# Performance work log

Measured on AMD Instinct MI355X. Metric: run time of the kernel, lower is better.

The kernel has to match this reference:

```python
import jax, jax.numpy as jnp
import numpy as np

SEQ, B, OBS, H, MLP_H, ACT = 64, 8192, 47, 64, 32, 12


def setup_inputs() -> dict:
    key = jax.random.key(0)
    ks = jax.random.split(key, 10)
    s = 1.0 / np.sqrt(H)
    return {
        "obs_seq": jax.random.normal(ks[0], (SEQ, B, OBS), dtype=jnp.float32),
        "h0": jnp.zeros((1, B, H), jnp.float32),
        "c0": jnp.zeros((1, B, H), jnp.float32),
        "W_ih": jax.random.uniform(ks[1], (4 * H, OBS), jnp.float32, -s, s),
        "W_hh": jax.random.uniform(ks[2], (4 * H, H), jnp.float32, -s, s),
        "b_ih": jax.random.uniform(ks[3], (4 * H,), jnp.float32, -s, s),
        "b_hh": jax.random.uniform(ks[4], (4 * H,), jnp.float32, -s, s),
        "W1": jax.random.uniform(ks[5], (MLP_H, H), jnp.float32, -s, s),
        "b1": jax.random.uniform(ks[6], (MLP_H,), jnp.float32, -s, s),
        "W2": jax.random.uniform(ks[7], (ACT, MLP_H), jnp.float32, -0.1, 0.1),
        "b2": jnp.zeros((ACT,), jnp.float32),
        "masks": jax.random.randint(ks[8], (SEQ, B), 0, 2, dtype=jnp.int32),
    }


def _lstm_scan(obs_seq, h0, c0, W_ih, W_hh, b_ih, b_hh, masks):
    b = b_ih + b_hh

    def step(carry, inp):
        h, c = carry  # (B,H)
        x, m = inp
        m = m.astype(h.dtype)[:, None]  # (B,1): 0 resets hidden state
        h = h * m
        c = c * m
        gates = x @ W_ih.T + h @ W_hh.T + b  # (B,4H), torch order i,f,g,o
        i, f, g, o = jnp.split(gates, 4, axis=-1)
        c = jax.nn.sigmoid(f) * c + jax.nn.sigmoid(i) * jnp.tanh(g)
        h = jax.nn.sigmoid(o) * jnp.tanh(c)
        return (h, c), h

    (h, c), outs = jax.lax.scan(step, (h0[0], c0[0]), (obs_seq, masks))
    return outs, h, c


def reference(obs_seq, h0, c0, W_ih, W_hh, b_ih, b_hh, W1, b1, W2, b2, masks):
    lstm_out, h, c = _lstm_scan(obs_seq, h0, c0, W_ih, W_hh, b_ih, b_hh, masks)
    means = jax.nn.elu(lstm_out @ W1.T + b1) @ W2.T + b2  # (SEQ,B,ACT)
    return means, h[None], c[None]
```

## Files before the change

### kernel.cpp

```cpp
#include <hip/hip_runtime.h>
#include <hip/hip_bf16.h>

#define SEQ   64
#define BATCH 8192
#define OBS   47
#define HID   64
#define MLPH  32
#define ACT   12

#define BT 16
#define NT 512
#define NWG (BATCH / BT)

#define XS0O 0
#define XS1O 2048
#define HM0O 4096
#define HM1O 6144
#define XA0O 8192
#define XA1O 24576
#define M2EO 40960
#define MSKO 43008
#define W1LO 47104
#define W2LO 51200
#define SMEM_BYTES 52224

#define L2E  1.4426950408889634f
#define L2E2 2.8853900817779268f

typedef __attribute__((ext_vector_type(8))) short short8;
typedef __attribute__((ext_vector_type(4))) float f32x4;

__device__ __forceinline__ ushort f2bf(float f) {
  union { float f; unsigned u; } v; v.f = f;
  return (ushort)((v.u + 0x7FFFu + ((v.u >> 16) & 1u)) >> 16);
}
__device__ __forceinline__ float ex2(float x) {
#if __has_builtin(__builtin_amdgcn_exp2f)
  return __builtin_amdgcn_exp2f(x);
#else
  return __expf(x * 0.6931471805599453f);
#endif
}
__device__ __forceinline__ float rcpx(float x) {
#if __has_builtin(__builtin_amdgcn_rcpf)
  return __builtin_amdgcn_rcpf(x);
#else
  return __fdividef(1.0f, x);
#endif
}
__device__ __forceinline__ float sigf(float x)     { return rcpx(1.0f + ex2(-L2E * x)); }
__device__ __forceinline__ float tanhfast(float x) { return __builtin_fmaf(-2.0f, rcpx(1.0f + ex2(L2E2 * x)), 1.0f); }
__device__ __forceinline__ unsigned cvtpk(float lo, float hi) {
  unsigned r; asm("v_cvt_pk_bf16_f32 %0, %1, %2" : "=v"(r) : "v"(lo), "v"(hi)); return r;
}

__device__ __forceinline__ void barrier_lgkm() {
  __builtin_amdgcn_sched_barrier(0);
  asm volatile("s_waitcnt lgkmcnt(0)" ::: "memory");
  __builtin_amdgcn_s_barrier();
  __builtin_amdgcn_sched_barrier(0);
}

__device__ __forceinline__ int swz (int r, int ks) { return (r * 128 + ks * 2) ^ ((r & 7) << 4); }
__device__ __forceinline__ int swzM(int r, int cs) { return (r * 64  + cs * 2) ^ ((r & 7) << 4); }

extern "C" __global__ void __launch_bounds__(NT, 4)
lstm_policy(const float* __restrict__ obs, const float* __restrict__ h0,
            const float* __restrict__ c0, const float* __restrict__ Wih,
            const float* __restrict__ Whh, const float* __restrict__ bih,
            const float* __restrict__ bhh, const float* __restrict__ W1,
            const float* __restrict__ b1, const float* __restrict__ W2,
            const float* __restrict__ b2, const int* __restrict__ masks,
            float* __restrict__ out)
{
  __shared__ __align__(16) char sm[SMEM_BYTES];
  const int tid  = threadIdx.x;
  const int b0   = blockIdx.x * BT;
  const int lane = tid & 63;
  const int w    = tid >> 6;
  const int lr   = lane & 15;
  const int lg   = lane >> 4;
  const int j    = (w & 3) * 16 + lr;

  int xsl[4];
  #pragma unroll
  for (int nf = 0; nf < 4; ++nf)
    xsl[nf] = (j << 8) + ((((lg * 4 + nf) ^ lr) & 15) << 4);

  for (int idx = tid; idx < 256; idx += NT)
    *(f32x4*)(sm + idx * 16) = (f32x4){0.f, 0.f, 0.f, 0.f};
  for (int idx = tid; idx < SEQ * BT; idx += NT) {
    int t = idx >> 4, r = idx & 15;
    *(float*)(sm + MSKO + idx * 4) = (float)masks[t * BATCH + b0 + r];
  }
  if (tid < 64) {
    int l = tid, llr = l & 15, llg = l >> 4;
    #pragma unroll
    for (int tt = 0; tt < 2; ++tt)
      #pragma unroll
      for (int kk = 0; kk < 2; ++kk) {
        short8 f;
        const float* src = W1 + (tt * 16 + llr) * HID + kk * 32 + llg * 8;
        #pragma unroll
        for (int e = 0; e < 8; ++e) f[e] = (short)f2bf(src[e]);
        *(short8*)(sm + W1LO + ((tt * 2 + kk) * 64 + l) * 16) = f;
      }
    short8 f2;
    #pragma unroll
    for (int e = 0; e < 8; ++e)
      f2[e] = (llr < ACT) ? (short)f2bf(W2[llr * MLPH + llg * 8 + e]) : (short)0;
    *(short8*)(sm + W2LO + l * 16) = f2;
  }
  __syncthreads();

  short8 wf[4][2];
  float biasg[4] = {0, 0, 0, 0};
  float creg[4] = {0, 0, 0, 0}, hlast[4] = {0, 0, 0, 0};
  int shw[4];
  #pragma unroll
  for (int q = 0; q < 4; ++q) shw[q] = swz(lg * 4 + q, j);

  if (w < 4) {
    #pragma unroll
    for (int nf = 0; nf < 4; ++nf) {
      int n = nf * 64 + j;
      #pragma unroll
      for (int kk = 0; kk < 2; ++kk) {
        const float* src = Whh + n * HID + kk * 32 + lg * 8;
        short8 f;
        #pragma unroll
        for (int e = 0; e < 8; ++e) f[e] = (short)f2bf(src[e]);
        wf[nf][kk] = f;
      }
    }
    #pragma unroll
    for (int q = 0; q < 4; ++q) {
      int r = lg * 4 + q;
      creg[q] = c0[(size_t)(b0 + r) * HID + j];
      *(ushort*)(sm + HM0O + shw[q]) = f2bf(h0[(size_t)(b0 + r) * HID + j]);
    }
  } else {
    #pragma unroll
    for (int nf = 0; nf < 4; ++nf) {
      int n = nf * 64 + j;
      biasg[nf] = bih[n] + bhh[n];
      #pragma unroll
      for (int kk = 0; kk < 2; ++kk) {
        short8 f;
        #pragma unroll
        for (int e = 0; e < 8; ++e) {
          int k = kk * 32 + lg * 8 + e;
          f[e] = (k < OBS) ? (short)f2bf(Wih[n * OBS + k]) : (short)0;
        }
        wf[nf][kk] = f;
      }
    }
  }

  float b1v0 = 0.f, b1v1 = 0.f, b2v = 0.f;
  if (w == 4) { b1v0 = b1[lr]; b1v1 = b1[16 + lr]; }
  if (w == 5) { b2v = (lr < ACT) ? b2[lr] : 0.f; }

  const int oidx = tid - 320;
  const bool oact = (w >= 5) && (oidx >= 0) && (oidx < 188);
  int a_obs[4] = {0, 0, 0, 0};
  f32x4 ovh = {0.f, 0.f, 0.f, 0.f};
  const float* obsp = obs;
  if (oact) {
    #pragma unroll
    for (int e = 0; e < 4; ++e) {
      int flat = oidx * 4 + e;
      int r = flat / OBS, k = flat - OBS * r;
      a_obs[e] = swz(r, k);
    }
    f32x4 v0 = *(const f32x4*)(obs + (size_t)b0 * OBS + oidx * 4);
    f32x4 v1 = *(const f32x4*)(obs + ((size_t)BATCH + b0) * OBS + oidx * 4);
    #pragma unroll
    for (int e = 0; e < 4; ++e) *(ushort*)(sm + XS0O + a_obs[e]) = f2bf(v0[e]);
    #pragma unroll
    for (int e = 0; e < 4; ++e) *(ushort*)(sm + XS1O + a_obs[e]) = f2bf(v1[e]);
    obsp = obs + ((size_t)2 * BATCH + b0) * OBS + oidx * 4;
    ovh = *(const f32x4*)(obsp);
    obsp += (size_t)BATCH * OBS;
  }
  __syncthreads();

  auto do_xgemm = [&](int B) {
    const int xsb = B ? XS1O : XS0O;
    const int xab = B ? XA1O : XA0O;
    short8 ax0 = *(const short8*)(sm + xsb + swz(lr, lg * 8));
    short8 ax1 = *(const short8*)(sm + xsb + swz(lr, 32 + lg * 8));
    #pragma unroll
    for (int nf = 0; nf < 4; ++nf) {
      f32x4 a = (f32x4){biasg[nf], biasg[nf], biasg[nf], biasg[nf]};
      a = __builtin_amdgcn_mfma_f32_16x16x32_bf16(ax0, wf[nf][0], a, 0, 0, 0);
      a = __builtin_amdgcn_mfma_f32_16x16x32_bf16(ax1, wf[nf][1], a, 0, 0, 0);
      *(f32x4*)(sm + xab + xsl[nf]) = a;
    }
  };

  if (w >= 4) do_xgemm(0);
  __syncthreads();

  auto do_mlp1 = [&](int TT, int HMB) {
    const int me = M2EO + (TT & 1) * 1024;
    short8 hf0 = *(const short8*)(sm + HMB + swz(lr, lg * 8));
    short8 hf1 = *(const short8*)(sm + HMB + swz(lr, 32 + lg * 8));
    f32x4 am0 = (f32x4){b1v0, b1v0, b1v0, b1v0};
    f32x4 am1 = (f32x4){b1v1, b1v1, b1v1, b1v1};
    short8 wA;
    wA = *(const short8*)(sm + W1LO + (0 * 64 + lane) * 16);
    am0 = __builtin_amdgcn_mfma_f32_16x16x32_bf16(hf0, wA, am0, 0, 0, 0);
    wA = *(const short8*)(sm + W1LO + (1 * 64 + lane) * 16);
    am0 = __builtin_amdgcn_mfma_f32_16x16x32_bf16(hf1, wA, am0, 0, 0, 0);
    wA = *(const short8*)(sm + W1LO + (2 * 64 + lane) * 16);
    am1 = __builtin_amdgcn_mfma_f32_16x16x32_bf16(hf0, wA, am1, 0, 0, 0);
    wA = *(const short8*)(sm + W1LO + (3 * 64 + lane) * 16);
    am1 = __builtin_amdgcn_mfma_f32_16x16x32_bf16(hf1, wA, am1, 0, 0, 0);
    #pragma unroll
    for (int q = 0; q < 4; ++q) {
      int r = lg * 4 + q;
      float v0 = am0[q], v1 = am1[q];
      float e0 = v0 > 0.f ? v0 : (ex2(L2E * v0) - 1.f);
      float e1 = v1 > 0.f ? v1 : (ex2(L2E * v1) - 1.f);
      unsigned u = cvtpk(e0, e1);
      *(ushort*)(sm + me + swzM(r, lr))      = (ushort)u;
      *(ushort*)(sm + me + swzM(r, 16 + lr)) = (ushort)(u >> 16);
    }
  };

  auto do_mlp2 = [&](int TT) {
    const int me = M2EO + (TT & 1) * 1024;
    f32x4 a2 = (f32x4){b2v, b2v, b2v, b2v};
    short8 ef  = *(const short8*)(sm + me + swzM(lr, lg * 8));
    short8 w2f = *(const short8*)(sm + W2LO + lane * 16);
    a2 = __builtin_amdgcn_mfma_f32_16x16x32_bf16(ef, w2f, a2, 0, 0, 0);
    if (lr < ACT) {
      float* op = out + ((size_t)TT * BATCH + b0 + lg * 4) * ACT + lr;
      #pragma unroll
      for (int q = 0; q < 4; ++q) op[q * ACT] = a2[q];
    }
  };

  auto do_step = [&](int P, int T) {
    if (w < 4) {
      __builtin_amdgcn_s_setprio(1);
      const int hmr = P ? HM1O : HM0O;
      const int hmw = P ? HM0O : HM1O;
      const int xar = P ? XA1O : XA0O;
      short8 ah0 = *(const short8*)(sm + hmr + swz(lr, lg * 8));
      short8 ah1 = *(const short8*)(sm + hmr + swz(lr, 32 + lg * 8));
      f32x4 xq0 = *(const f32x4*)(sm + xar + xsl[0]);
      f32x4 xq1 = *(const f32x4*)(sm + xar + xsl[1]);
      f32x4 xq2 = *(const f32x4*)(sm + xar + xsl[2]);
      f32x4 xq3 = *(const f32x4*)(sm + xar + xsl[3]);
      const f32x4 z = {0.f, 0.f, 0.f, 0.f};
      f32x4 pa0 = __builtin_amdgcn_mfma_f32_16x16x32_bf16(ah0, wf[0][0], z, 0, 0, 0);
      f32x4 pa1 = __builtin_amdgcn_mfma_f32_16x16x32_bf16(ah0, wf[1][0], z, 0, 0, 0);
      f32x4 pa2 = __builtin_amdgcn_mfma_f32_16x16x32_bf16(ah0, wf[2][0], z, 0, 0, 0);
      f32x4 pa3 = __builtin_amdgcn_mfma_f32_16x16x32_bf16(ah0, wf[3][0], z, 0, 0, 0);
      f32x4 pb0 = __builtin_amdgcn_mfma_f32_16x16x32_bf16(ah1, wf[0][1], z, 0, 0, 0);
      f32x4 pb1 = __builtin_amdgcn_mfma_f32_16x16x32_bf16(ah1, wf[1][1], z, 0, 0, 0);
      f32x4 pb2 = __builtin_amdgcn_mfma_f32_16x16x32_bf16(ah1, wf[2][1], z, 0, 0, 0);
      f32x4 pb3 = __builtin_amdgcn_mfma_f32_16x16x32_bf16(ah1, wf[3][1], z, 0, 0, 0);

      f32x4 mc = *(const f32x4*)(sm + MSKO + (T << 6) + (lg << 4));
      f32x4 g0 = xq0 + mc * (pa0 + pb0);
      f32x4 g1 = xq1 + mc * (pa1 + pb1);
      f32x4 g2 = xq2 + mc * (pa2 + pb2);
      f32x4 g3 = xq3 + mc * (pa3 + pb3);

      float hq[4];
      #pragma unroll
      for (int q = 0; q < 4; ++q) {
        float iv = sigf(g0[q]);
        float fv = sigf(g1[q]);
        float gv = tanhfast(g2[q]);
        float ov = sigf(g3[q]);
        float c  = fv * (creg[q] * mc[q]) + iv * gv;
        float h  = ov * tanhfast(c);
        creg[q]  = c;
        hlast[q] = h;
        hq[q]    = h;
      }
      unsigned u01 = cvtpk(hq[0], hq[1]);
      unsigned u23 = cvtpk(hq[2], hq[3]);
      *(ushort*)(sm + hmw + shw[0]) = (ushort)u01;
      *(ushort*)(sm + hmw + shw[1]) = (ushort)(u01 >> 16);
      *(ushort*)(sm + hmw + shw[2]) = (ushort)u23;
      *(ushort*)(sm + hmw + shw[3]) = (ushort)(u23 >> 16);
      __builtin_amdgcn_s_setprio(0);
    } else {
      if (T + 1 < SEQ) do_xgemm(P ^ 1);
      if (w == 4) {
        if (T > 0) do_mlp1(T - 1, P ? HM1O : HM0O);
      } else if (w == 5 && T > 1) {
        do_mlp2(T - 2);
      }
      if (oact) {
        f32x4 ovn = ovh;
        if (T + 3 < SEQ) { ovn = *(const f32x4*)(obsp); }
        obsp += (size_t)BATCH * OBS;
        if (T + 2 < SEQ) {
          const int xsw = P ? XS1O : XS0O;
          unsigned p0 = cvtpk(ovh[0], ovh[1]), p1 = cvtpk(ovh[2], ovh[3]);
          *(ushort*)(sm + xsw + a_obs[0]) = (ushort)p0;
          *(ushort*)(sm + xsw + a_obs[1]) = (ushort)(p0 >> 16);
          *(ushort*)(sm + xsw + a_obs[2]) = (ushort)p1;
          *(ushort*)(sm + xsw + a_obs[3]) = (ushort)(p1 >> 16);
        }
        ovh = ovn;
      }
    }
    barrier_lgkm();
  };

  for (int t = 0; t < SEQ; t += 2) {
    do_step(0, t);
    do_step(1, t + 1);
  }
  if (w == 4) do_mlp1(63, HM0O);
  else if (w == 5) do_mlp2(62);
  barrier_lgkm();
  if (w == 5) do_mlp2(63);

  if (w < 4) {
    float* hout = out + (size_t)SEQ * BATCH * ACT;
    float* cout = hout + (size_t)BATCH * HID;
    #pragma unroll
    for (int q = 0; q < 4; ++q) {
      int r = lg * 4 + q;
      hout[(size_t)(b0 + r) * HID + j] = hlast[q];
      cout[(size_t)(b0 + r) * HID + j] = creg[q];
    }
  }
}

extern "C" void kernel_launch(void* const* d_in, const int* in_sizes, int n_in,
                              void* d_out, int out_size, void* d_ws, size_t ws_size,
                              hipStream_t stream) {
  (void)in_sizes; (void)n_in; (void)d_ws; (void)ws_size; (void)out_size;
  lstm_policy<<<dim3(NWG), dim3(NT), 0, stream>>>(
      (const float*)d_in[0], (const float*)d_in[1], (const float*)d_in[2],
      (const float*)d_in[3], (const float*)d_in[4], (const float*)d_in[5],
      (const float*)d_in[6], (const float*)d_in[7], (const float*)d_in[8],
      (const float*)d_in[9], (const float*)d_in[10], (const int*)d_in[11],
      (float*)d_out);
}
```

Before: 106.8 us.

## Merge helper waves into recurrent waves, halving workgroup size to 256 threads

New measurement: 109.5 us. 1.03x slower.

```diff
diff --git a/kernel.cpp b/kernel.cpp
--- a/kernel.cpp
+++ b/kernel.cpp
@@ -9,7 +9,7 @@
 #define ACT   12
 
 #define BT 16
-#define NT 512
+#define NT 256
 #define NWG (BATCH / BT)
 
 #define XS0O 0
@@ -64,7 +64,7 @@
 __device__ __forceinline__ int swz (int r, int ks) { return (r * 128 + ks * 2) ^ ((r & 7) << 4); }
 __device__ __forceinline__ int swzM(int r, int cs) { return (r * 64  + cs * 2) ^ ((r & 7) << 4); }
 
-extern "C" __global__ void __launch_bounds__(NT, 4)
+extern "C" __global__ void __launch_bounds__(NT, 2)
 lstm_policy(const float* __restrict__ obs, const float* __restrict__ h0,
             const float* __restrict__ c0, const float* __restrict__ Wih,
             const float* __restrict__ Whh, const float* __restrict__ bih,
@@ -80,7 +80,7 @@
   const int w    = tid >> 6;
   const int lr   = lane & 15;
   const int lg   = lane >> 4;
-  const int j    = (w & 3) * 16 + lr;
+  const int j    = w * 16 + lr;
 
   int xsl[4];
   #pragma unroll
@@ -113,56 +113,47 @@
   }
   __syncthreads();
 
-  short8 wf[4][2];
-  float biasg[4] = {0, 0, 0, 0};
+  short8 whh[4][2], wih[4][2];
+  float biasg[4];
   float creg[4] = {0, 0, 0, 0}, hlast[4] = {0, 0, 0, 0};
   int shw[4];
   #pragma unroll
   for (int q = 0; q < 4; ++q) shw[q] = swz(lg * 4 + q, j);
 
-  if (w < 4) {
-    #pragma unroll
-    for (int nf = 0; nf < 4; ++nf) {
-      int n = nf * 64 + j;
+  #pragma unroll
+  for (int nf = 0; nf < 4; ++nf) {
+    int n = nf * 64 + j;
+    biasg[nf] = bih[n] + bhh[n];
+    #pragma unroll
+    for (int kk = 0; kk < 2; ++kk) {
+      const float* src = Whh + n * HID + kk * 32 + lg * 8;
+      short8 f;
       #pragma unroll
-      for (int kk = 0; kk < 2; ++kk) {
-        const float* src = Whh + n * HID + kk * 32 + lg * 8;
-        short8 f;
-        #pragma unroll
-        for (int e = 0; e < 8; ++e) f[e] = (short)f2bf(src[e]);
-        wf[nf][kk] = f;
+      for (int e = 0; e < 8; ++e) f[e] = (short)f2bf(src[e]);
+      whh[nf][kk] = f;
+      short8 g;
+      #pragma unroll
+      for (int e = 0; e < 8; ++e) {
+        int k = kk * 32 + lg * 8 + e;
+        g[e] = (k < OBS) ? (short)f2bf(Wih[n * OBS + k]) : (short)0;
       }
-    }
-    #pragma unroll
-    for (int q = 0; q < 4; ++q) {
-      int r = lg * 4 + q;
-      creg[q] = c0[(size_t)(b0 + r) * HID + j];
-      *(ushort*)(sm + HM0O + shw[q]) = f2bf(h0[(size_t)(b0 + r) * HID + j]);
-    }
-  } else {
-    #pragma unroll
-    for (int nf = 0; nf < 4; ++nf) {
-      int n = nf * 64 + j;
-      biasg[nf] = bih[n] + bhh[n];
-      #pragma unroll
-      for (int kk = 0; kk < 2; ++kk) {
-        short8 f;
-        #pragma unroll
-        for (int e = 0; e < 8; ++e) {
-          int k = kk * 32 + lg * 8 + e;
-          f[e] = (k < OBS) ? (short)f2bf(Wih[n * OBS + k]) : (short)0;
-        }
-        wf[nf][kk] = f;
-      }
-    }
-  }
-
-  float b1v0 = 0.f, b1v1 = 0.f, b2v = 0.f;
-  if (w == 4) { b1v0 = b1[lr]; b1v1 = b1[16 + lr]; }
-  if (w == 5) { b2v = (lr < ACT) ? b2[lr] : 0.f; }
-
-  const int oidx = tid - 320;
-  const bool oact = (w >= 5) && (oidx >= 0) && (oidx < 188);
+      wih[nf][kk] = g;
+    }
+  }
+  #pragma unroll
+  for (int q = 0; q < 4; ++q) {
+    int r = lg * 4 + q;
+    creg[q] = c0[(size_t)(b0 + r) * HID + j];
+    *(ushort*)(sm + HM0O + shw[q]) = f2bf(h0[(size_t)(b0 + r) * HID + j]);
+  }
+
+  float b1v = 0.f, b2v = 0.f;
+  if (w == 0) b1v = b1[lr];
+  if (w == 1) b1v = b1[16 + lr];
+  if (w == 2) b2v = (lr < ACT) ? b2[lr] : 0.f;
+
+  const int oidx = tid - 64;
+  const bool oact = (oidx >= 0) && (oidx < 188);
   int a_obs[4] = {0, 0, 0, 0};
   f32x4 ovh = {0.f, 0.f, 0.f, 0.f};
   const float* obsp = obs;
@@ -193,40 +184,38 @@
     #pragma unroll
     for (int nf = 0; nf < 4; ++nf) {
       f32x4 a = (f32x4){biasg[nf], biasg[nf], biasg[nf], biasg[nf]};
-      a = __builtin_amdgcn_mfma_f32_16x16x32_bf16(ax0, wf[nf][0], a, 0, 0, 0);
-      a = __builtin_amdgcn_mfma_f32_16x16x32_bf16(ax1, wf[nf][1], a, 0, 0, 0);
+      a = __builtin_amdgcn_mfma_f32_16x16x32_bf16(ax0, wih[nf][0], a, 0, 0, 0);
+      a = __builtin_amdgcn_mfma_f32_16x16x32_bf16(ax1, wih[nf][1], a, 0, 0, 0);
       *(f32x4*)(sm + xab + xsl[nf]) = a;
     }
   };
 
-  if (w >= 4) do_xgemm(0);
+  do_xgemm(0);
   __syncthreads();
 
-  auto do_mlp1 = [&](int TT, int HMB) {
+  auto do_mlp1h = [&](int TT, int HMB, int half) {
     const int me = M2EO + (TT & 1) * 1024;
     short8 hf0 = *(const short8*)(sm + HMB + swz(lr, lg * 8));
     short8 hf1 = *(const short8*)(sm + HMB + swz(lr, 32 + lg * 8));
-    f32x4 am0 = (f32x4){b1v0, b1v0, b1v0, b1v0};
-    f32x4 am1 = (f32x4){b1v1, b1v1, b1v1, b1v1};
+    f32x4 am = (f32x4){b1v, b1v, b1v, b1v};
     short8 wA;
-    wA = *(const short8*)(sm + W1LO + (0 * 64 + lane) * 16);
-    am0 = __builtin_amdgcn_mfma_f32_16x16x32_bf16(hf0, wA, am0, 0, 0, 0);
-    wA = *(const short8*)(sm + W1LO + (1 * 64 + lane) * 16);
-    am0 = __builtin_amdgcn_mfma_f32_16x16x32_bf16(hf1, wA, am0, 0, 0, 0);
-    wA = *(const short8*)(sm + W1LO + (2 * 64 + lane) * 16);
-    am1 = __builtin_amdgcn_mfma_f32_16x16x32_bf16(hf0, wA, am1, 0, 0, 0);
-    wA = *(const short8*)(sm + W1LO + (3 * 64 + lane) * 16);
-    am1 = __builtin_amdgcn_mfma_f32_16x16x32_bf16(hf1, wA, am1, 0, 0, 0);
+    wA = *(const short8*)(sm + W1LO + ((half * 2 + 0) * 64 + lane) * 16);
+    am = __builtin_amdgcn_mfma_f32_16x16x32_bf16(hf0, wA, am, 0, 0, 0);
+    wA = *(const short8*)(sm + W1LO + ((half * 2 + 1) * 64 + lane) * 16);
+    am = __builtin_amdgcn_mfma_f32_16x16x32_bf16(hf1, wA, am, 0, 0, 0);
+    float e[4];
     #pragma unroll
     for (int q = 0; q < 4; ++q) {
-      int r = lg * 4 + q;
-      float v0 = am0[q], v1 = am1[q];
-      float e0 = v0 > 0.f ? v0 : (ex2(L2E * v0) - 1.f);
-      float e1 = v1 > 0.f ? v1 : (ex2(L2E * v1) - 1.f);
-      unsigned u = cvtpk(e0, e1);
-      *(ushort*)(sm + me + swzM(r, lr))      = (ushort)u;
-      *(ushort*)(sm + me + swzM(r, 16 + lr)) = (ushort)(u >> 16);
-    }
+      float v = am[q];
+      e[q] = v > 0.f ? v : (ex2(L2E * v) - 1.f);
+    }
+    unsigned u01 = cvtpk(e[0], e[1]);
+    unsigned u23 = cvtpk(e[2], e[3]);
+    const int c = half * 16 + lr;
+    *(ushort*)(sm + me + swzM(lg * 4 + 0, c)) = (ushort)u01;
+    *(ushort*)(sm + me + swzM(lg * 4 + 1, c)) = (ushort)(u01 >> 16);
+    *(ushort*)(sm + me + swzM(lg * 4 + 2, c)) = (ushort)u23;
+    *(ushort*)(sm + me + swzM(lg * 4 + 3, c)) = (ushort)(u23 >> 16);
   };
 
   auto do_mlp2 = [&](int TT) {
@@ -243,74 +232,73 @@
   };
 
   auto do_step = [&](int P, int T) {
-    if (w < 4) {
-      __builtin_amdgcn_s_setprio(1);
-      const int hmr = P ? HM1O : HM0O;
-      const int hmw = P ? HM0O : HM1O;
-      const int xar = P ? XA1O : XA0O;
-      short8 ah0 = *(const short8*)(sm + hmr + swz(lr, lg * 8));
-      short8 ah1 = *(const short8*)(sm + hmr + swz(lr, 32 + lg * 8));
-      f32x4 xq0 = *(const f32x4*)(sm + xar + xsl[0]);
-      f32x4 xq1 = *(const f32x4*)(sm + xar + xsl[1]);
-      f32x4 xq2 = *(const f32x4*)(sm + xar + xsl[2]);
-      f32x4 xq3 = *(const f32x4*)(sm + xar + xsl[3]);
-      const f32x4 z = {0.f, 0.f, 0.f, 0.f};
-      f32x4 pa0 = __builtin_amdgcn_mfma_f32_16x16x32_bf16(ah0, wf[0][0], z, 0, 0, 0);
-      f32x4 pa1 = __builtin_amdgcn_mfma_f32_16x16x32_bf16(ah0, wf[1][0], z, 0, 0, 0);
-      f32x4 pa2 = __builtin_amdgcn_mfma_f32_16x16x32_bf16(ah0, wf[2][0], z, 0, 0, 0);
-      f32x4 pa3 = __builtin_amdgcn_mfma_f32_16x16x32_bf16(ah0, wf[3][0], z, 0, 0, 0);
-      f32x4 pb0 = __builtin_amdgcn_mfma_f32_16x16x32_bf16(ah1, wf[0][1], z, 0, 0, 0);
-      f32x4 pb1 = __builtin_amdgcn_mfma_f32_16x16x32_bf16(ah1, wf[1][1], z, 0, 0, 0);
-      f32x4 pb2 = __builtin_amdgcn_mfma_f32_16x16x32_bf16(ah1, wf[2][1], z, 0, 0, 0);
-      f32x4 pb3 = __builtin_amdgcn_mfma_f32_16x16x32_bf16(ah1, wf[3][1], z, 0, 0, 0);
-
-      f32x4 mc = *(const f32x4*)(sm + MSKO + (T << 6) + (lg << 4));
-      f32x4 g0 = xq0 + mc * (pa0 + pb0);
-      f32x4 g1 = xq1 + mc * (pa1 + pb1);
-      f32x4 g2 = xq2 + mc * (pa2 + pb2);
-      f32x4 g3 = xq3 + mc * (pa3 + pb3);
-
-      float hq[4];
-      #pragma unroll
-      for (int q = 0; q < 4; ++q) {
-        float iv = sigf(g0[q]);
-        float fv = sigf(g1[q]);
-        float gv = tanhfast(g2[q]);
-        float ov = sigf(g3[q]);
-        float c  = fv * (creg[q] * mc[q]) + iv * gv;
-        float h  = ov * tanhfast(c);
-        creg[q]  = c;
-        hlast[q] = h;
-        hq[q]    = h;
+    const int hmr = P ? HM1O : HM0O;
+    const int hmw = P ? HM0O : HM1O;
+    const int xar = P ? XA1O : XA0O;
+    short8 ah0 = *(const short8*)(sm + hmr + swz(lr, lg * 8));
+    short8 ah1 = *(const short8*)(sm + hmr + swz(lr, 32 + lg * 8));
+    f32x4 xq0 = *(const f32x4*)(sm + xar + xsl[0]);
+    f32x4 xq1 = *(const f32x4*)(sm + xar + xsl[1]);
+    f32x4 xq2 = *(const f32x4*)(sm + xar + xsl[2]);
+    f32x4 xq3 = *(const f32x4*)(sm + xar + xsl[3]);
+    const f32x4 z = {0.f, 0.f, 0.f, 0.f};
+    f32x4 pa0 = __builtin_amdgcn_mfma_f32_16x16x32_bf16(ah0, whh[0][0], z, 0, 0, 0);
+    f32x4 pa1 = __builtin_amdgcn_mfma_f32_16x16x32_bf16(ah0, whh[1][0], z, 0, 0, 0);
+    f32x4 pa2 = __builtin_amdgcn_mfma_f32_16x16x32_bf16(ah0, whh[2][0], z, 0, 0, 0);
+    f32x4 pa3 = __builtin_amdgcn_mfma_f32_16x16x32_bf16(ah0, whh[3][0], z, 0, 0, 0);
+    f32x4 pb0 = __builtin_amdgcn_mfma_f32_16x16x32_bf16(ah1, whh[0][1], z, 0, 0, 0);
+    f32x4 pb1 = __builtin_amdgcn_mfma_f32_16x16x32_bf16(ah1, whh[1][1], z, 0, 0, 0);
+    f32x4 pb2 = __builtin_amdgcn_mfma_f32_16x16x32_bf16(ah1, whh[2][1], z, 0, 0, 0);
+    f32x4 pb3 = __builtin_amdgcn_mfma_f32_16x16x32_bf16(ah1, whh[3][1], z, 0, 0, 0);
+
+    f32x4 mc = *(const f32x4*)(sm + MSKO + (T << 6) + (lg << 4));
+    f32x4 g0 = xq0 + mc * (pa0 + pb0);
+    f32x4 g1 = xq1 + mc * (pa1 + pb1);
+    f32x4 g2 = xq2 + mc * (pa2 + pb2);
+    f32x4 g3 = xq3 + mc * (pa3 + pb3);
+
+    float hq[4];
+    #pragma unroll
+    for (int q = 0; q < 4; ++q) {
+      float iv = sigf(g0[q]);
+      float fv = sigf(g1[q]);
+      float gv = tanhfast(g2[q]);
+      float ov = sigf(g3[q]);
+      float c  = fv * (creg[q] * mc[q]) + iv * gv;
+      float h  = ov * tanhfast(c);
+      creg[q]  = c;
+      hlast[q] = h;
+      hq[q]    = h;
+    }
+    unsigned u01 = cvtpk(hq[0], hq[1]);
+    unsigned u23 = cvtpk(hq[2], hq[3]);
+    *(ushort*)(sm + hmw + shw[0]) = (ushort)u01;
+    *(ushort*)(sm + hmw + shw[1]) = (ushort)(u01 >> 16);
+    *(ushort*)(sm + hmw + shw[2]) = (ushort)u23;
+    *(ushort*)(sm + hmw + shw[3]) = (ushort)(u23 >> 16);
+
+    if (T + 1 < SEQ) do_xgemm(P ^ 1);
+
+    if (w == 0) {
+      if (T > 0) do_mlp1h(T - 1, hmr, 0);
+    } else if (w == 1) {
+      if (T > 0) do_mlp1h(T - 1, hmr, 1);
+    } else if (w == 2) {
+      if (T > 1) do_mlp2(T - 2);
+    }
+    if (oact) {
+      f32x4 ovn = ovh;
+      if (T + 3 < SEQ) { ovn = *(const f32x4*)(obsp); }
+      obsp += (size_t)BATCH * OBS;
+      if (T + 2 < SEQ) {
+        const int xsw = P ? XS1O : XS0O;
+        unsigned p0 = cvtpk(ovh[0], ovh[1]), p1 = cvtpk(ovh[2], ovh[3]);
+        *(ushort*)(sm + xsw + a_obs[0]) = (ushort)p0;
+        *(ushort*)(sm + xsw + a_obs[1]) = (ushort)(p0 >> 16);
+        *(ushort*)(sm + xsw + a_obs[2]) = (ushort)p1;
+        *(ushort*)(sm + xsw + a_obs[3]) = (ushort)(p1 >> 16);
       }
-      unsigned u01 = cvtpk(hq[0], hq[1]);
-      unsigned u23 = cvtpk(hq[2], hq[3]);
-      *(ushort*)(sm + hmw + shw[0]) = (ushort)u01;
-      *(ushort*)(sm + hmw + shw[1]) = (ushort)(u01 >> 16);
-      *(ushort*)(sm + hmw + shw[2]) = (ushort)u23;
-      *(ushort*)(sm + hmw + shw[3]) = (ushort)(u23 >> 16);
-      __builtin_amdgcn_s_setprio(0);
-    } else {
-      if (T + 1 < SEQ) do_xgemm(P ^ 1);
-      if (w == 4) {
-        if (T > 0) do_mlp1(T - 1, P ? HM1O : HM0O);
-      } else if (w == 5 && T > 1) {
-        do_mlp2(T - 2);
-      }
-      if (oact) {
-        f32x4 ovn = ovh;
-        if (T + 3 < SEQ) { ovn = *(const f32x4*)(obsp); }
-        obsp += (size_t)BATCH * OBS;
-        if (T + 2 < SEQ) {
-          const int xsw = P ? XS1O : XS0O;
-          unsigned p0 = cvtpk(ovh[0], ovh[1]), p1 = cvtpk(ovh[2], ovh[3]);
-          *(ushort*)(sm + xsw + a_obs[0]) = (ushort)p0;
-          *(ushort*)(sm + xsw + a_obs[1]) = (ushort)(p0 >> 16);
-          *(ushort*)(sm + xsw + a_obs[2]) = (ushort)p1;
-          *(ushort*)(sm + xsw + a_obs[3]) = (ushort)(p1 >> 16);
-        }
-        ovh = ovn;
-      }
+      ovh = ovn;
     }
     barrier_lgkm();
   };
@@ -319,12 +307,13 @@
     do_step(0, t);
     do_step(1, t + 1);
   }
-  if (w == 4) do_mlp1(63, HM0O);
-  else if (w == 5) do_mlp2(62);
+  if (w == 0)      do_mlp1h(63, HM0O, 0);
+  else if (w == 1) do_mlp1h(63, HM0O, 1);
+  else if (w == 2) do_mlp2(62);
   barrier_lgkm();
-  if (w == 5) do_mlp2(63);
-
-  if (w < 4) {
+  if (w == 2) do_mlp2(63);
+
+  {
     float* hout = out + (size_t)SEQ * BATCH * ACT;
     float* cout = hout + (size_t)BATCH * HID;
     #pragma unroll
```
